# Kernel optimization log

Measured on AMD Instinct MI355X. Metric: run time of the kernel, lower is better.

Reference implementation:

```python
import jax, jax.numpy as jnp
import numpy as np

EPS = 1e-6
BETA = 0.25
NVQ_W = 1.0


def _mlp(h, params):
    # Linear + ReLU on all but last layer (dropout=0, bn=False)
    n = len(params)
    for i, (w, b) in enumerate(params):
        h = h @ w + b
        if i < n - 1:
            h = jax.nn.relu(h)
    return h


def _kuma_ab(a_raw, b_raw):
    return jax.nn.softplus(a_raw) + EPS, jax.nn.softplus(b_raw) + EPS


def _kuma_h(z, a, b):
    x = jnp.clip(jax.nn.sigmoid(z), EPS, 1.0 - EPS)
    inner = jnp.clip(1.0 - x ** a, EPS, 1.0)
    y = 1.0 - inner ** b
    return jnp.clip(y, EPS, 1.0 - EPS)


def _kuma_h_inv(y, a, b):
    y = jnp.clip(y, EPS, 1.0 - EPS)
    omy = jnp.clip(1.0 - y, EPS, 1.0)
    inner = jnp.clip(1.0 - omy ** (1.0 / b), EPS, 1.0 - EPS)
    x = jnp.clip(inner ** (1.0 / a), EPS, 1.0 - EPS)
    return jnp.log(x / (1.0 - x))


def _rq(z, codebooks):
    # Residual VQ: per level, squared-L2 nearest code (argmin), straight-through,
    # codebook + beta*commitment loss. sk_epsilon=0 -> Sinkhorn skipped.
    sg = jax.lax.stop_gradient
    residual = z
    x_q = jnp.zeros_like(z)
    losses, idx_list = [], []
    for l in range(codebooks.shape[0]):
        cb = codebooks[l]  # [K, D]
        d = (jnp.sum(residual * residual, -1, keepdims=True)
             + jnp.sum(cb * cb, -1)
             - 2.0 * residual @ cb.T)  # [B, K]
        idx = jnp.argmin(d, axis=-1)  # [B]
        q = cb[idx]  # [B, D]
        codebook_loss = jnp.mean((q - sg(residual)) ** 2)
        commit_loss = jnp.mean((sg(q) - residual) ** 2)
        losses.append(codebook_loss + BETA * commit_loss)
        q_st = residual + sg(q - residual)  # straight-through
        residual = residual - q_st
        x_q = x_q + q_st
        idx_list.append(idx)
    return x_q, jnp.mean(jnp.stack(losses)), jnp.stack(idx_list, axis=-1)


def _forward(x, enc, dec, codebooks, a_raw, b_raw):
    z = _mlp(x, enc)
    a, b = _kuma_ab(a_raw, b_raw)
    z_prime = _kuma_h(z, a, b)
    zq_prime, rq_loss, indices = _rq(z_prime, codebooks)
    z_q = _kuma_h_inv(zq_prime, a, b)
    z_recon = _kuma_h_inv(z_prime, a, b)
    nvq_loss = jnp.mean((z_recon - z) ** 2)
    total_quant_loss = rq_loss + NVQ_W * nvq_loss
    out = _mlp(z_q, dec)
    return out, total_quant_loss, indices


def setup_inputs() -> dict:
    key = jax.random.key(0)
    ks = jax.random.split(key, 16)
    B, IN = 16384, 768
    enc_dims = [768, 2048, 1024, 512, 128]
    dec_dims = enc_dims[::-1]

    def lin(k, din, dout):
        w = jax.random.normal(k, (din, dout), jnp.float32) * (1.0 / np.sqrt(din))
        return w, jnp.zeros((dout,), jnp.float32)

    inp = {"x": jax.random.normal(ks[0], (B, IN), jnp.float32)}
    for i in range(4):
        w, b = lin(ks[1 + i], enc_dims[i], enc_dims[i + 1])
        inp[f"enc_w{i}"], inp[f"enc_b{i}"] = w, b
        w, b = lin(ks[5 + i], dec_dims[i], dec_dims[i + 1])
        inp[f"dec_w{i}"], inp[f"dec_b{i}"] = w, b
    inp["codebooks"] = jax.random.normal(ks[9], (4, 256, 128), jnp.float32)
    inp["a_raw"] = jnp.zeros((128,), jnp.float32)
    inp["b_raw"] = jnp.zeros((128,), jnp.float32)
    return inp


def reference(x, enc_w0, enc_b0, enc_w1, enc_b1, enc_w2, enc_b2, enc_w3, enc_b3,
              dec_w0, dec_b0, dec_w1, dec_b1, dec_w2, dec_b2, dec_w3, dec_b3,
              codebooks, a_raw, b_raw):
    enc = [(enc_w0, enc_b0), (enc_w1, enc_b1), (enc_w2, enc_b2), (enc_w3, enc_b3)]
    dec = [(dec_w0, dec_b0), (dec_w1, dec_b1), (dec_w2, dec_b2), (dec_w3, dec_b3)]
    return _forward(x, enc, dec, codebooks, a_raw, b_raw)
```

## Files before the change

kernel.cpp:

```cpp
#include <hip/hip_runtime.h>
#include <math.h>

#define EPS_F 1e-6f
#define ONE_M_EPS (1.0f - 1e-6f)

typedef __attribute__((ext_vector_type(8))) short s16x8;
typedef __attribute__((ext_vector_type(8))) _Float16 f16x8;
typedef __attribute__((ext_vector_type(4))) float f32x4;

__device__ __forceinline__ ushort f2bf(float f) {
    union { float f; unsigned u; } v; v.f = f;
    unsigned u = v.u;
    return (ushort)((u + 0x7FFFu + ((u >> 16) & 1u)) >> 16);
}
__device__ __forceinline__ float bf2f(ushort h) {
    union { unsigned u; float f; } v; v.u = ((unsigned)h) << 16;
    return v.f;
}
__device__ __forceinline__ void split2h(float x, ushort& h, ushort& m) {
    union { _Float16 f; ushort u; } a, b;
    a.f = (_Float16)x;
    float r = x - (float)a.f;
    b.f = (_Float16)r;
    h = a.u; m = b.u;
}

#define GLL16(srcp, dstp)                                                     \
    __builtin_amdgcn_global_load_lds(                                         \
        (const __attribute__((address_space(1))) void*)(srcp),                \
        (__attribute__((address_space(3))) void*)(dstp), 16, 0, 0)

__device__ __forceinline__ int swz_k(int row, int k) { return k ^ ((row >> 1) & 3); }

template<bool RELU, int OUT2>
__global__ __launch_bounds__(256) void gemm_mfma_split2(
    const ushort* __restrict__ Ah, const ushort* __restrict__ Am,
    const ushort* __restrict__ Wh, const ushort* __restrict__ Wm,
    const float* __restrict__ bias,
    void* __restrict__ C0, void* __restrict__ C1,
    int M, int N, int K)
{
    __shared__ __align__(16) ushort As[2][2][128 * 32];
    __shared__ __align__(16) ushort Bs[2][2][128 * 32];

    const int tid  = threadIdx.x;
    const int lane = tid & 63;
    const int w    = tid >> 6;
    const int wm   = (w >> 1) * 64;
    const int wn   = (w & 1) * 64;
    const int bm   = blockIdx.x * 128;
    const int bn   = blockIdx.y * 128;

    f32x4 acc[4][4];
#pragma unroll
    for (int i = 0; i < 4; i++)
#pragma unroll
        for (int j = 0; j < 4; j++) acc[i][j] = f32x4{0.f, 0.f, 0.f, 0.f};

    const int c0 = (w * 2) * 64 + lane;
    const int c1 = (w * 2 + 1) * 64 + lane;
    const int r0 = c0 >> 2, k0e = swz_k(r0, c0 & 3) * 8;
    const int r1 = c1 >> 2, k1e = swz_k(r1, c1 & 3) * 8;

    const size_t a_off0 = (size_t)(bm + r0) * K + k0e;
    const size_t a_off1 = (size_t)(bm + r1) * K + k1e;
    const size_t b_off0 = (size_t)(bn + r0) * K + k0e;
    const size_t b_off1 = (size_t)(bn + r1) * K + k1e;
    const int d0 = (w * 2) * 512;
    const int d1 = d0 + 512;

    const ushort* Ap[2] = {Ah, Am};
    const ushort* Wp[2] = {Wh, Wm};

    const int fm  = lane & 15;
    const int fkb = lane >> 4;
    const int NT  = K >> 5;

#pragma unroll
    for (int p = 0; p < 2; p++) {
        GLL16(Ap[p] + a_off0, &As[0][p][d0]);
        GLL16(Ap[p] + a_off1, &As[0][p][d1]);
        GLL16(Wp[p] + b_off0, &Bs[0][p][d0]);
        GLL16(Wp[p] + b_off1, &Bs[0][p][d1]);
    }

    int cur = 0;
    for (int kt = 0; kt < NT; kt++) {
        if (kt + 1 < NT) {
            const int kk = (kt + 1) << 5;
#pragma unroll
            for (int p = 0; p < 2; p++) {
                GLL16(Ap[p] + a_off0 + kk, &As[cur ^ 1][p][d0]);
                GLL16(Ap[p] + a_off1 + kk, &As[cur ^ 1][p][d1]);
                GLL16(Wp[p] + b_off0 + kk, &Bs[cur ^ 1][p][d0]);
                GLL16(Wp[p] + b_off1 + kk, &Bs[cur ^ 1][p][d1]);
            }
            asm volatile("s_waitcnt vmcnt(8)" ::: "memory");
        } else {
            asm volatile("s_waitcnt vmcnt(0)" ::: "memory");
        }
        __builtin_amdgcn_s_barrier();
        asm volatile("" ::: "memory");

        f16x8 af[2][4];
#pragma unroll
        for (int p = 0; p < 2; p++)
#pragma unroll
            for (int i = 0; i < 4; i++) {
                const int row = wm + i * 16 + fm;
                af[p][i] = *reinterpret_cast<const f16x8*>(
                    &As[cur][p][row * 32 + swz_k(row, fkb) * 8]);
            }
        f16x8 bf0[4], bf1[4];
#pragma unroll
        for (int j = 0; j < 4; j++) {
            const int row = wn + j * 16 + fm;
            bf0[j] = *reinterpret_cast<const f16x8*>(&Bs[cur][0][row * 32 + swz_k(row, fkb) * 8]);
            bf1[j] = *reinterpret_cast<const f16x8*>(&Bs[cur][1][row * 32 + swz_k(row, fkb) * 8]);
        }

        __builtin_amdgcn_s_setprio(1);
#pragma unroll
        for (int i = 0; i < 4; i++)
#pragma unroll
            for (int j = 0; j < 4; j++) {
                acc[i][j] = __builtin_amdgcn_mfma_f32_16x16x32_f16(af[0][i], bf0[j], acc[i][j], 0, 0, 0);
                acc[i][j] = __builtin_amdgcn_mfma_f32_16x16x32_f16(af[0][i], bf1[j], acc[i][j], 0, 0, 0);
                acc[i][j] = __builtin_amdgcn_mfma_f32_16x16x32_f16(af[1][i], bf0[j], acc[i][j], 0, 0, 0);
            }
        __builtin_amdgcn_s_setprio(0);
        asm volatile("" ::: "memory");
        __builtin_amdgcn_s_barrier();
        cur ^= 1;
    }

#pragma unroll
    for (int j = 0; j < 4; j++) {
        const int coln = bn + wn + j * 16 + fm;
        const float bv = bias[coln];
#pragma unroll
        for (int i = 0; i < 4; i++) {
            const int row0 = bm + wm + i * 16 + (lane >> 4) * 4;
#pragma unroll
            for (int r = 0; r < 4; r++) {
                float o = acc[i][j][r] + bv;
                if (RELU) o = fmaxf(o, 0.f);
                const size_t idx = (size_t)(row0 + r) * N + coln;
                if (OUT2) {
                    ushort h, m;
                    split2h(o, h, m);
                    ((ushort*)C0)[idx] = h;
                    ((ushort*)C1)[idx] = m;
                } else {
                    ((float*)C0)[idx] = o;
                }
            }
        }
    }
}

template<bool RELU, bool OUT_BF16>
__global__ __launch_bounds__(256) void gemm_mfma_bt(
    const ushort* __restrict__ A, const ushort* __restrict__ WT,
    const float* __restrict__ bias, void* __restrict__ Cv,
    int M, int N, int K)
{
    __shared__ __align__(16) ushort As[2][128 * 32];
    __shared__ __align__(16) ushort Bs[2][128 * 32];

    const int tid  = threadIdx.x;
    const int lane = tid & 63;
    const int w    = tid >> 6;
    const int wm   = (w >> 1) * 64;
    const int wn   = (w & 1) * 64;
    const int bm   = blockIdx.x * 128;
    const int bn   = blockIdx.y * 128;

    f32x4 acc[4][4];
#pragma unroll
    for (int i = 0; i < 4; i++)
#pragma unroll
        for (int j = 0; j < 4; j++) acc[i][j] = f32x4{0.f, 0.f, 0.f, 0.f};

    const int c0 = (w * 2) * 64 + lane;
    const int c1 = (w * 2 + 1) * 64 + lane;
    const int r0 = c0 >> 2, k0e = swz_k(r0, c0 & 3) * 8;
    const int r1 = c1 >> 2, k1e = swz_k(r1, c1 & 3) * 8;

    const ushort* a_src0 = A  + (size_t)(bm + r0) * K + k0e;
    const ushort* a_src1 = A  + (size_t)(bm + r1) * K + k1e;
    const ushort* b_src0 = WT + (size_t)(bn + r0) * K + k0e;
    const ushort* b_src1 = WT + (size_t)(bn + r1) * K + k1e;
    const int d0 = (w * 2) * 512;
    const int d1 = d0 + 512;

    const int fm  = lane & 15;
    const int fkb = lane >> 4;
    const int NT  = K >> 5;

    GLL16(a_src0, &As[0][d0]);
    GLL16(a_src1, &As[0][d1]);
    GLL16(b_src0, &Bs[0][d0]);
    GLL16(b_src1, &Bs[0][d1]);

    int cur = 0;
    for (int kt = 0; kt < NT; kt++) {
        if (kt + 1 < NT) {
            const int kk = (kt + 1) << 5;
            GLL16(a_src0 + kk, &As[cur ^ 1][d0]);
            GLL16(a_src1 + kk, &As[cur ^ 1][d1]);
            GLL16(b_src0 + kk, &Bs[cur ^ 1][d0]);
            GLL16(b_src1 + kk, &Bs[cur ^ 1][d1]);
            asm volatile("s_waitcnt vmcnt(4)" ::: "memory");
        } else {
            asm volatile("s_waitcnt vmcnt(0)" ::: "memory");
        }
        __builtin_amdgcn_s_barrier();
        asm volatile("" ::: "memory");

        s16x8 af[4], bfr[4];
#pragma unroll
        for (int i = 0; i < 4; i++) {
            const int row = wm + i * 16 + fm;
            af[i] = *reinterpret_cast<const s16x8*>(&As[cur][row * 32 + swz_k(row, fkb) * 8]);
        }
#pragma unroll
        for (int j = 0; j < 4; j++) {
            const int row = wn + j * 16 + fm;
            bfr[j] = *reinterpret_cast<const s16x8*>(&Bs[cur][row * 32 + swz_k(row, fkb) * 8]);
        }

        __builtin_amdgcn_s_setprio(1);
#pragma unroll
        for (int i = 0; i < 4; i++)
#pragma unroll
            for (int j = 0; j < 4; j++)
                acc[i][j] = __builtin_amdgcn_mfma_f32_16x16x32_bf16(
                    af[i], bfr[j], acc[i][j], 0, 0, 0);
        __builtin_amdgcn_s_setprio(0);
        asm volatile("" ::: "memory");
        __builtin_amdgcn_s_barrier();
        cur ^= 1;
    }

#pragma unroll
    for (int j = 0; j < 4; j++) {
        const int coln = bn + wn + j * 16 + fm;
        const float bv = bias[coln];
#pragma unroll
        for (int i = 0; i < 4; i++) {
            const int row0 = bm + wm + i * 16 + (lane >> 4) * 4;
#pragma unroll
            for (int r = 0; r < 4; r++) {
                float o = acc[i][j][r] + bv;
                if (RELU) o = fmaxf(o, 0.f);
                if (OUT_BF16)
                    ((ushort*)Cv)[(size_t)(row0 + r) * N + coln] = f2bf(o);
                else
                    ((float*)Cv)[(size_t)(row0 + r) * N + coln] = o;
            }
        }
    }
}

__global__ __launch_bounds__(256) void transpose_to_bf16(
    const float* __restrict__ W, ushort* __restrict__ WT, int K, int N)
{
    __shared__ float t[32][33];
    const int kb = blockIdx.x * 32, nb = blockIdx.y * 32;
    const int tx = threadIdx.x & 31, ty = threadIdx.x >> 5;
#pragma unroll
    for (int i = ty; i < 32; i += 8)
        t[i][tx] = W[(size_t)(kb + i) * N + nb + tx];
    __syncthreads();
#pragma unroll
    for (int i = ty; i < 32; i += 8)
        WT[(size_t)(nb + i) * K + kb + tx] = f2bf(t[tx][i]);
}

__global__ __launch_bounds__(256) void transpose_split_f16(
    const float* __restrict__ W, ushort* __restrict__ TH,
    ushort* __restrict__ TM, int K, int N)
{
    __shared__ float t[32][33];
    const int kb = blockIdx.x * 32, nb = blockIdx.y * 32;
    const int tx = threadIdx.x & 31, ty = threadIdx.x >> 5;
#pragma unroll
    for (int i = ty; i < 32; i += 8)
        t[i][tx] = W[(size_t)(kb + i) * N + nb + tx];
    __syncthreads();
#pragma unroll
    for (int i = ty; i < 32; i += 8) {
        ushort h, m;
        split2h(t[tx][i], h, m);
        const size_t idx = (size_t)(nb + i) * K + kb + tx;
        TH[idx] = h; TM[idx] = m;
    }
}

__global__ __launch_bounds__(256) void split_plane2_kernel(
    const float* __restrict__ X, ushort* __restrict__ H,
    ushort* __restrict__ M, size_t n)
{
    size_t i = (size_t)blockIdx.x * 256 + threadIdx.x;
    if (i >= n) return;
    ushort h, m;
    split2h(X[i], h, m);
    H[i] = h; M[i] = m;
}

__global__ __launch_bounds__(128) void prep_cb_kernel(
    const float* __restrict__ cb, float* __restrict__ cbT, float* __restrict__ cnorm)
{
    int b = blockIdx.x;
    int d = threadIdx.x;
    float v = cb[(size_t)b * 128 + d];
    int l = b >> 8, c = b & 255;
    cbT[((size_t)l * 128 + d) * 256 + c] = v;
    float s = v * v;
#pragma unroll
    for (int off = 32; off > 0; off >>= 1) s += __shfl_down(s, off);
    __shared__ float ps[2];
    if ((d & 63) == 0) ps[d >> 6] = s;
    __syncthreads();
    if (d == 0) cnorm[b] = ps[0] + ps[1];
}

__device__ __forceinline__ float softplusf(float x) {
    return (x > 20.f) ? x : log1pf(expf(x));
}

__global__ void kuma_ab_init(const float* __restrict__ a_raw, const float* __restrict__ b_raw,
                             float* __restrict__ kp)
{
    int t = threadIdx.x;
    if (t < 128) {
        float a = softplusf(a_raw[t]) + EPS_F;
        float b = softplusf(b_raw[t]) + EPS_F;
        kp[t] = a;
        kp[128 + t] = b;
        kp[256 + t] = 1.f / a;
        kp[384 + t] = 1.f / b;
    }
}

__global__ __launch_bounds__(256) void kuma_h_kernel(
    const float* __restrict__ z, const float* __restrict__ kp,
    float* __restrict__ zp, int n)
{
    int i = blockIdx.x * 256 + threadIdx.x;
    if (i >= n) return;
    int col = i & 127;
    float a = kp[col], b = kp[128 + col];
    float zv = z[i];
    float x = 1.f / (1.f + expf(-zv));
    x = fminf(fmaxf(x, EPS_F), ONE_M_EPS);
    float inner = 1.f - powf(x, a);
    inner = fminf(fmaxf(inner, EPS_F), 1.f);
    float y = 1.f - powf(inner, b);
    y = fminf(fmaxf(y, EPS_F), ONE_M_EPS);
    zp[i] = y;
}

__global__ __launch_bounds__(64) void rq_kernel2(
    const float* __restrict__ zp, const float* __restrict__ cb,
    const float* __restrict__ cbT, const float* __restrict__ cnorm,
    float* __restrict__ xq, float* __restrict__ idx_out,
    float* __restrict__ prq, int bid0, int nRq)
{
    __shared__ float res[4][128];

    const int t = threadIdx.x;
    const int row0 = blockIdx.x * 4;

#pragma unroll
    for (int j = 0; j < 8; j++) {
        int e = t + j * 64;
        res[e >> 7][e & 127] = zp[(size_t)row0 * 128 + e];
    }

    float lsum[4];

#pragma unroll 1
    for (int l = 0; l < 4; l++) {
        const float* cT = cbT + (size_t)l * 32768;

        float acc[4][4];
#pragma unroll
        for (int r = 0; r < 4; r++)
#pragma unroll
            for (int cc = 0; cc < 4; cc++) acc[r][cc] = 0.f;

        float pc[16];
#pragma unroll
        for (int dd = 0; dd < 4; dd++)
#pragma unroll
            for (int cc = 0; cc < 4; cc++)
                pc[dd * 4 + cc] = cT[dd * 256 + cc * 64 + t];

#pragma unroll 2
        for (int d = 0; d < 128; d += 4) {
            float nc[16];
            if (d < 124) {
#pragma unroll
                for (int dd = 0; dd < 4; dd++)
#pragma unroll
                    for (int cc = 0; cc < 4; cc++)
                        nc[dd * 4 + cc] = cT[(d + 4 + dd) * 256 + cc * 64 + t];
            }
#pragma unroll
            for (int r = 0; r < 4; r++) {
                float4 rv = *reinterpret_cast<const float4*>(&res[r][d]);
#pragma unroll
                for (int cc = 0; cc < 4; cc++) {
                    acc[r][cc] += rv.x * pc[cc] + rv.y * pc[4 + cc]
                                + rv.z * pc[8 + cc] + rv.w * pc[12 + cc];
                }
            }
#pragma unroll
            for (int k = 0; k < 16; k++) pc[k] = nc[k];
        }

        float cn[4];
#pragma unroll
        for (int cc = 0; cc < 4; cc++) cn[cc] = cnorm[l * 256 + cc * 64 + t];

        int bidx0, bidx1, bidx2, bidx3;
#pragma unroll
        for (int r = 0; r < 4; r++) {
            float dmin = cn[0] - 2.f * acc[r][0];
            int imin = t;
#pragma unroll
            for (int cc = 1; cc < 4; cc++) {
                float dv = cn[cc] - 2.f * acc[r][cc];
                if (dv < dmin) { dmin = dv; imin = cc * 64 + t; }
            }
#pragma unroll
            for (int off = 1; off < 64; off <<= 1) {
                float d2 = __shfl_xor(dmin, off);
                int i2 = __shfl_xor(imin, off);
                if (d2 < dmin || (d2 == dmin && i2 < imin)) { dmin = d2; imin = i2; }
            }
            if (r == 0) bidx0 = imin;
            else if (r == 1) bidx1 = imin;
            else if (r == 2) bidx2 = imin;
            else bidx3 = imin;
            if (t == 0) idx_out[(size_t)(row0 + r) * 4 + l] = (float)imin;
        }

        float s = 0.f;
#pragma unroll
        for (int j = 0; j < 8; j++) {
            const int r = j >> 1;
            const int d = (j & 1) * 64 + t;
            const int bi = (r == 0) ? bidx0 : (r == 1) ? bidx1 : (r == 2) ? bidx2 : bidx3;
            float q = cb[((size_t)(l * 256) + bi) * 128 + d];
            float nr = res[r][d] - q;
            res[r][d] = nr;
            s += nr * nr;
        }
        lsum[l] = s;
    }

#pragma unroll
    for (int j = 0; j < 8; j++) {
        int e = t + j * 64;
        xq[(size_t)row0 * 128 + e] = zp[(size_t)row0 * 128 + e] - res[e >> 7][e & 127];
    }

#pragma unroll
    for (int l = 0; l < 4; l++) {
        float s = lsum[l];
#pragma unroll
        for (int off = 32; off > 0; off >>= 1) s += __shfl_down(s, off);
        if (t == 0) prq[(size_t)l * nRq + bid0 + blockIdx.x] = s;
    }
}

__device__ __forceinline__ float kuma_h_inv_f(float y, float ia, float ib) {
    y = fminf(fmaxf(y, EPS_F), ONE_M_EPS);
    float omy = fminf(fmaxf(1.f - y, EPS_F), 1.f);
    float inner = fminf(fmaxf(1.f - powf(omy, ib), EPS_F), ONE_M_EPS);
    float x = fminf(fmaxf(powf(inner, ia), EPS_F), ONE_M_EPS);
    return logf(x / (1.f - x));
}

__global__ __launch_bounds__(256) void zq_nvq_kernel(
    const float* __restrict__ xq, const float* __restrict__ zp,
    const float* __restrict__ z, const float* __restrict__ kp,
    float* __restrict__ zq, ushort* __restrict__ zq16,
    float* __restrict__ pnvq, int bid0, int n)
{
    int i = blockIdx.x * 256 + threadIdx.x;
    float ds = 0.f;
    if (i < n) {
        int col = i & 127;
        float ia = kp[256 + col], ib = kp[384 + col];
        float xv = xq[i];
        float zpv = zp[i];
        float zv = z[i];
        float zr = kuma_h_inv_f(zpv, ia, ib);
        float d = zr - zv;
        ds = d * d;
        float zqv = kuma_h_inv_f(xv, ia, ib);
        zq[i] = zqv;
        zq16[i] = f2bf(zqv);
    }
#pragma unroll
    for (int off = 32; off > 0; off >>= 1) ds += __shfl_down(ds, off);
    __shared__ float ps[4];
    if ((threadIdx.x & 63) == 0) ps[threadIdx.x >> 6] = ds;
    __syncthreads();
    if (threadIdx.x == 0)
        pnvq[bid0 + blockIdx.x] = ps[0] + ps[1] + ps[2] + ps[3];
}

__global__ __launch_bounds__(256) void finalize_kernel(
    const float* __restrict__ prq, const float* __restrict__ pnvq,
    int nRqAll, int nNvq, float* __restrict__ out_loss)
{
    const int t = threadIdx.x;
    float srq = 0.f, snvq = 0.f;
    for (int i = t; i < nRqAll; i += 256) srq += prq[i];
    for (int i = t; i < nNvq; i += 256) snvq += pnvq[i];
#pragma unroll
    for (int off = 32; off > 0; off >>= 1) {
        srq += __shfl_down(srq, off);
        snvq += __shfl_down(snvq, off);
    }
    __shared__ float pr[4], pn[4];
    if ((t & 63) == 0) { pr[t >> 6] = srq; pn[t >> 6] = snvq; }
    __syncthreads();
    if (t == 0) {
        const float inv = 1.f / (16384.f * 128.f);
        float rq = (pr[0] + pr[1] + pr[2] + pr[3]);
        float nv = (pn[0] + pn[1] + pn[2] + pn[3]);
        out_loss[0] = 0.3125f * rq * inv + nv * inv;
    }
}

extern "C" void kernel_launch(void* const* d_in, const int* in_sizes, int n_in,
                              void* d_out, int out_size, void* d_ws, size_t ws_size,
                              hipStream_t stream)
{
    constexpr int B = 16384;

    const float* x = (const float*)d_in[0];
    const float* enc_w[4]; const float* enc_b[4];
    const float* dec_w[4]; const float* dec_b[4];
    for (int i = 0; i < 4; i++) {
        enc_w[i] = (const float*)d_in[1 + 4 * i];
        enc_b[i] = (const float*)d_in[2 + 4 * i];
        dec_w[i] = (const float*)d_in[3 + 4 * i];
        dec_b[i] = (const float*)d_in[4 + 4 * i];
    }
    const float* cb    = (const float*)d_in[17];
    const float* a_raw = (const float*)d_in[18];
    const float* b_raw = (const float*)d_in[19];

    size_t avail = ws_size / 4;
    const size_t fixed_f = 6547008;
    int R = 16384;
    while (R > 256 && (size_t)R * 3520 + fixed_f > avail) R >>= 1;

    float* ws    = (float*)d_ws;
    float* slotA = ws;
    float* slotB = slotA + (size_t)R * 1024;
    float* zb    = slotB + (size_t)R * 2048;
    float* zpb   = zb  + (size_t)R * 128;
    float* xqb   = zpb + (size_t)R * 128;
    float* zq16f = xqb + (size_t)R * 128;
    float* fixp  = zq16f + (size_t)R * 64;

    ushort* ew = (ushort*)fixp;
    ushort* e0h = ew;            ushort* e0m = e0h + 1572864;
    ushort* e1h = e0m + 1572864; ushort* e1m = e1h + 2097152;
    ushort* e2h = e1m + 2097152; ushort* e2m = e2h + 524288;
    ushort* e3h = e2m + 524288;  ushort* e3m = e3h + 65536;
    ushort* wt0 = e3m + 65536;
    ushort* wt1 = wt0 + 65536;
    ushort* wt2 = wt1 + 524288;
    ushort* wt3 = wt2 + 2097152;
    float* cbT   = (float*)(wt3 + 1572864);
    float* cnorm = cbT + 4 * 128 * 256;
    float* kp    = cnorm + 4 * 256;
    float* prq   = kp + 512;
    float* pnvq  = prq + 16384;

    ushort* zq16 = (ushort*)zq16f;

    ushort* xH  = (ushort*)slotA;  ushort* xM  = xH  + (size_t)R * 768;
    ushort* h0H = (ushort*)slotB;  ushort* h0M = h0H + (size_t)R * 2048;
    ushort* h1H = (ushort*)slotA;  ushort* h1M = h1H + (size_t)R * 1024;
    ushort* h2H = (ushort*)slotB;  ushort* h2M = h2H + (size_t)R * 512;

    ushort* dA = (ushort*)slotB;
    ushort* dB = (ushort*)(slotB + (size_t)R * 256);
    ushort* dC = (ushort*)slotA;

    float* out      = (float*)d_out;
    float* out_loss = out + (size_t)B * 768;
    float* out_idx  = out_loss + 1;

    prep_cb_kernel<<<1024, 128, 0, stream>>>(cb, cbT, cnorm);
    kuma_ab_init<<<1, 128, 0, stream>>>(a_raw, b_raw, kp);
    transpose_split_f16<<<dim3( 768/32, 2048/32), 256, 0, stream>>>(enc_w[0], e0h, e0m,  768, 2048);
    transpose_split_f16<<<dim3(2048/32, 1024/32), 256, 0, stream>>>(enc_w[1], e1h, e1m, 2048, 1024);
    transpose_split_f16<<<dim3(1024/32,  512/32), 256, 0, stream>>>(enc_w[2], e2h, e2m, 1024,  512);
    transpose_split_f16<<<dim3( 512/32,  128/32), 256, 0, stream>>>(enc_w[3], e3h, e3m,  512,  128);
    transpose_to_bf16<<<dim3(128/32,  512/32), 256, 0, stream>>>(dec_w[0], wt0,  128,  512);
    transpose_to_bf16<<<dim3(512/32, 1024/32), 256, 0, stream>>>(dec_w[1], wt1,  512, 1024);
    transpose_to_bf16<<<dim3(1024/32,2048/32), 256, 0, stream>>>(dec_w[2], wt2, 1024, 2048);
    transpose_to_bf16<<<dim3(2048/32, 768/32), 256, 0, stream>>>(dec_w[3], wt3, 2048,  768);

    const int nc = B / R;
    const int nRq = B / 4;
    const int rqPerChunk = R / 4;
    const int nvqPerChunk = (R * 128) / 256;
    for (int c = 0; c < nc; c++) {
        const size_t base = (size_t)c * R;
        const float* xc = x + base * 768;
        float* outc = out + base * 768;
        float* idxc = out_idx + base * 4;

        {
            size_t n = (size_t)R * 768;
            split_plane2_kernel<<<(unsigned)((n + 255) / 256), 256, 0, stream>>>(xc, xH, xM, n);
        }

        gemm_mfma_split2<true , 1><<<dim3(R/128, 16), 256, 0, stream>>>(
            xH, xM, e0h, e0m, enc_b[0], h0H, h0M, R, 2048, 768);
        gemm_mfma_split2<true , 1><<<dim3(R/128,  8), 256, 0, stream>>>(
            h0H, h0M, e1h, e1m, enc_b[1], h1H, h1M, R, 1024, 2048);
        gemm_mfma_split2<true , 1><<<dim3(R/128,  4), 256, 0, stream>>>(
            h1H, h1M, e2h, e2m, enc_b[2], h2H, h2M, R,  512, 1024);
        gemm_mfma_split2<false, 0><<<dim3(R/128,  1), 256, 0, stream>>>(
            h2H, h2M, e3h, e3m, enc_b[3], zb, nullptr, R, 128, 512);

        kuma_h_kernel<<<(R * 128) / 256, 256, 0, stream>>>(zb, kp, zpb, R * 128);
        rq_kernel2<<<rqPerChunk, 64, 0, stream>>>(zpb, cb, cbT, cnorm, xqb, idxc,
                                                  prq, c * rqPerChunk, nRq);
        zq_nvq_kernel<<<nvqPerChunk, 256, 0, stream>>>(xqb, zpb, zb, kp, xqb, zq16,
                                                       pnvq, c * nvqPerChunk, R * 128);

        gemm_mfma_bt<true , true ><<<dim3(R/128,  4), 256, 0, stream>>>(zq16, wt0, dec_b[0], dA, R,  512,  128);
        gemm_mfma_bt<true , true ><<<dim3(R/128,  8), 256, 0, stream>>>(dA,   wt1, dec_b[1], dB, R, 1024,  512);
        gemm_mfma_bt<true , true ><<<dim3(R/128, 16), 256, 0, stream>>>(dB,   wt2, dec_b[2], dC, R, 2048, 1024);
        gemm_mfma_bt<false, false><<<dim3(R/128,  6), 256, 0, stream>>>(dC,   wt3, dec_b[3], outc, R,  768, 2048);
    }

    finalize_kernel<<<1, 256, 0, stream>>>(prq, pnvq, 4 * nRq, B * 128 / 256, out_loss);
}
```

Baseline: 913.5 us.

## Add triple-buffered 128x256 pipelined GEMM for encoder and decoder layers

```diff
diff --git a/kernel.cpp b/kernel.cpp
--- a/kernel.cpp
+++ b/kernel.cpp
@@ -31,6 +31,170 @@
         (__attribute__((address_space(3))) void*)(dstp), 16, 0, 0)
 
 __device__ __forceinline__ int swz_k(int row, int k) { return k ^ ((row >> 1) & 3); }
+
+template<int NWAIT> __device__ __forceinline__ void vmwait() {
+    if constexpr (NWAIT == 12)      asm volatile("s_waitcnt vmcnt(12)" ::: "memory");
+    else if constexpr (NWAIT == 6)  asm volatile("s_waitcnt vmcnt(6)"  ::: "memory");
+    else if constexpr (NWAIT == 3)  asm volatile("s_waitcnt vmcnt(3)"  ::: "memory");
+    else                            asm volatile("s_waitcnt vmcnt(0)"  ::: "memory");
+}
+
+template<int PLANES, bool RELU, int OUTMODE>
+__global__ __launch_bounds__(512) void gemm_pipe(
+    const ushort* __restrict__ A0, const ushort* __restrict__ A1,
+    const ushort* __restrict__ W0, const ushort* __restrict__ W1,
+    const float* __restrict__ bias,
+    void* __restrict__ C0, void* __restrict__ C1,
+    int M, int N, int K)
+{
+    __shared__ __align__(16) ushort As[3][PLANES][4096];
+    __shared__ __align__(16) ushort Bs[3][PLANES][8192];
+
+    const int tid  = threadIdx.x;
+    const int lane = tid & 63;
+    const int w    = tid >> 6;
+    const int wm   = (w >> 2) * 64;
+    const int wn   = (w & 3) * 64;
+    const int bm   = blockIdx.x * 128;
+    const int bn   = blockIdx.y * 256;
+
+    f32x4 acc[4][4];
+#pragma unroll
+    for (int i = 0; i < 4; i++)
+#pragma unroll
+        for (int j = 0; j < 4; j++) acc[i][j] = f32x4{0.f, 0.f, 0.f, 0.f};
+
+    const int sr   = tid >> 2;
+    const int skc  = swz_k(sr, tid & 3) * 8;
+    const int br1r = 128 + sr;
+    const int bk1  = swz_k(br1r, tid & 3) * 8;
+
+    const size_t a_off  = (size_t)(bm + sr)   * K + skc;
+    const size_t b_off0 = (size_t)(bn + sr)   * K + skc;
+    const size_t b_off1 = (size_t)(bn + br1r) * K + bk1;
+    const int ud = w * 512;
+
+    const ushort* Ap[2] = {A0, A1};
+    const ushort* Wp[2] = {W0, W1};
+
+    const int fm  = lane & 15;
+    const int fkb = lane >> 4;
+    const int NT  = K >> 5;
+
+    auto STAGE = [&](int kk, int b) {
+#pragma unroll
+        for (int p = 0; p < PLANES; p++) {
+            GLL16(Ap[p] + a_off  + kk, &As[b][p][ud]);
+            GLL16(Wp[p] + b_off0 + kk, &Bs[b][p][ud]);
+            GLL16(Wp[p] + b_off1 + kk, &Bs[b][p][4096 + ud]);
+        }
+    };
+
+    STAGE(0, 0);
+    STAGE(32, 1);
+
+    int cur = 0;
+    for (int kt = 0; kt < NT; kt++) {
+        __builtin_amdgcn_s_barrier();
+        asm volatile("" ::: "memory");
+        if (kt + 2 < NT) {
+            const int sb = (cur == 0) ? 2 : cur - 1;
+            STAGE((kt + 2) << 5, sb);
+            vmwait<6 * PLANES>();
+        } else if (kt + 1 < NT) {
+            vmwait<3 * PLANES>();
+        } else {
+            vmwait<0>();
+        }
+        asm volatile("" ::: "memory");
+
+        if constexpr (PLANES == 2) {
+            f16x8 a[2][4], b[2][4];
+#pragma unroll
+            for (int p = 0; p < 2; p++)
+#pragma unroll
+                for (int i = 0; i < 4; i++) {
+                    const int row = wm + i * 16 + fm;
+                    a[p][i] = *reinterpret_cast<const f16x8*>(
+                        &As[cur][p][row * 32 + swz_k(row, fkb) * 8]);
+                }
+#pragma unroll
+            for (int p = 0; p < 2; p++)
+#pragma unroll
+                for (int j = 0; j < 4; j++) {
+                    const int row = wn + j * 16 + fm;
+                    b[p][j] = *reinterpret_cast<const f16x8*>(
+                        &Bs[cur][p][row * 32 + swz_k(row, fkb) * 8]);
+                }
+            __builtin_amdgcn_s_setprio(1);
+#pragma unroll
+            for (int i = 0; i < 4; i++)
+#pragma unroll
+                for (int j = 0; j < 4; j++)
+                    acc[i][j] = __builtin_amdgcn_mfma_f32_16x16x32_f16(a[0][i], b[0][j], acc[i][j], 0, 0, 0);
+#pragma unroll
+            for (int i = 0; i < 4; i++)
+#pragma unroll
+                for (int j = 0; j < 4; j++)
+                    acc[i][j] = __builtin_amdgcn_mfma_f32_16x16x32_f16(a[0][i], b[1][j], acc[i][j], 0, 0, 0);
+#pragma unroll
+            for (int i = 0; i < 4; i++)
+#pragma unroll
+                for (int j = 0; j < 4; j++)
+                    acc[i][j] = __builtin_amdgcn_mfma_f32_16x16x32_f16(a[1][i], b[0][j], acc[i][j], 0, 0, 0);
+            __builtin_amdgcn_s_setprio(0);
+        } else {
+            s16x8 a[4], b[4];
+#pragma unroll
+            for (int i = 0; i < 4; i++) {
+                const int row = wm + i * 16 + fm;
+                a[i] = *reinterpret_cast<const s16x8*>(
+                    &As[cur][0][row * 32 + swz_k(row, fkb) * 8]);
+            }
+#pragma unroll
+            for (int j = 0; j < 4; j++) {
+                const int row = wn + j * 16 + fm;
+                b[j] = *reinterpret_cast<const s16x8*>(
+                    &Bs[cur][0][row * 32 + swz_k(row, fkb) * 8]);
+            }
+            __builtin_amdgcn_s_setprio(1);
+#pragma unroll
+            for (int i = 0; i < 4; i++)
+#pragma unroll
+                for (int j = 0; j < 4; j++)
+                    acc[i][j] = __builtin_amdgcn_mfma_f32_16x16x32_bf16(a[i], b[j], acc[i][j], 0, 0, 0);
+            __builtin_amdgcn_s_setprio(0);
+        }
+        asm volatile("" ::: "memory");
+        cur = (cur == 2) ? 0 : cur + 1;
+    }
+
+#pragma unroll
+    for (int j = 0; j < 4; j++) {
+        const int coln = bn + wn + j * 16 + fm;
+        const float bv = bias[coln];
+#pragma unroll
+        for (int i = 0; i < 4; i++) {
+            const int row0 = bm + wm + i * 16 + (lane >> 4) * 4;
+#pragma unroll
+            for (int r = 0; r < 4; r++) {
+                float o = acc[i][j][r] + bv;
+                if (RELU) o = fmaxf(o, 0.f);
+                const size_t idx = (size_t)(row0 + r) * N + coln;
+                if constexpr (OUTMODE == 1) {
+                    ushort h, m;
+                    split2h(o, h, m);
+                    ((ushort*)C0)[idx] = h;
+                    ((ushort*)C1)[idx] = m;
+                } else if constexpr (OUTMODE == 2) {
+                    ((ushort*)C0)[idx] = f2bf(o);
+                } else {
+                    ((float*)C0)[idx] = o;
+                }
+            }
+        }
+    }
+}
 
 template<bool RELU, int OUT2>
 __global__ __launch_bounds__(256) void gemm_mfma_split2(
@@ -154,110 +318,6 @@
                 } else {
                     ((float*)C0)[idx] = o;
                 }
-            }
-        }
-    }
-}
-
-template<bool RELU, bool OUT_BF16>
-__global__ __launch_bounds__(256) void gemm_mfma_bt(
-    const ushort* __restrict__ A, const ushort* __restrict__ WT,
-    const float* __restrict__ bias, void* __restrict__ Cv,
-    int M, int N, int K)
-{
-    __shared__ __align__(16) ushort As[2][128 * 32];
-    __shared__ __align__(16) ushort Bs[2][128 * 32];
-
-    const int tid  = threadIdx.x;
-    const int lane = tid & 63;
-    const int w    = tid >> 6;
-    const int wm   = (w >> 1) * 64;
-    const int wn   = (w & 1) * 64;
-    const int bm   = blockIdx.x * 128;
-    const int bn   = blockIdx.y * 128;
-
-    f32x4 acc[4][4];
-#pragma unroll
-    for (int i = 0; i < 4; i++)
-#pragma unroll
-        for (int j = 0; j < 4; j++) acc[i][j] = f32x4{0.f, 0.f, 0.f, 0.f};
-
-    const int c0 = (w * 2) * 64 + lane;
-    const int c1 = (w * 2 + 1) * 64 + lane;
-    const int r0 = c0 >> 2, k0e = swz_k(r0, c0 & 3) * 8;
-    const int r1 = c1 >> 2, k1e = swz_k(r1, c1 & 3) * 8;
-
-    const ushort* a_src0 = A  + (size_t)(bm + r0) * K + k0e;
-    const ushort* a_src1 = A  + (size_t)(bm + r1) * K + k1e;
-    const ushort* b_src0 = WT + (size_t)(bn + r0) * K + k0e;
-    const ushort* b_src1 = WT + (size_t)(bn + r1) * K + k1e;
-    const int d0 = (w * 2) * 512;
-    const int d1 = d0 + 512;
-
-    const int fm  = lane & 15;
-    const int fkb = lane >> 4;
-    const int NT  = K >> 5;
-
-    GLL16(a_src0, &As[0][d0]);
-    GLL16(a_src1, &As[0][d1]);
-    GLL16(b_src0, &Bs[0][d0]);
-    GLL16(b_src1, &Bs[0][d1]);
-
-    int cur = 0;
-    for (int kt = 0; kt < NT; kt++) {
-        if (kt + 1 < NT) {
-            const int kk = (kt + 1) << 5;
-            GLL16(a_src0 + kk, &As[cur ^ 1][d0]);
-            GLL16(a_src1 + kk, &As[cur ^ 1][d1]);
-            GLL16(b_src0 + kk, &Bs[cur ^ 1][d0]);
-            GLL16(b_src1 + kk, &Bs[cur ^ 1][d1]);
-            asm volatile("s_waitcnt vmcnt(4)" ::: "memory");
-        } else {
-            asm volatile("s_waitcnt vmcnt(0)" ::: "memory");
-        }
-        __builtin_amdgcn_s_barrier();
-        asm volatile("" ::: "memory");
-
-        s16x8 af[4], bfr[4];
-#pragma unroll
-        for (int i = 0; i < 4; i++) {
-            const int row = wm + i * 16 + fm;
-            af[i] = *reinterpret_cast<const s16x8*>(&As[cur][row * 32 + swz_k(row, fkb) * 8]);
-        }
-#pragma unroll
-        for (int j = 0; j < 4; j++) {
-            const int row = wn + j * 16 + fm;
-            bfr[j] = *reinterpret_cast<const s16x8*>(&Bs[cur][row * 32 + swz_k(row, fkb) * 8]);
-        }
-
-        __builtin_amdgcn_s_setprio(1);
-#pragma unroll
-        for (int i = 0; i < 4; i++)
-#pragma unroll
-            for (int j = 0; j < 4; j++)
-                acc[i][j] = __builtin_amdgcn_mfma_f32_16x16x32_bf16(
-                    af[i], bfr[j], acc[i][j], 0, 0, 0);
-        __builtin_amdgcn_s_setprio(0);
-        asm volatile("" ::: "memory");
-        __builtin_amdgcn_s_barrier();
-        cur ^= 1;
-    }
-
-#pragma unroll
-    for (int j = 0; j < 4; j++) {
-        const int coln = bn + wn + j * 16 + fm;
-        const float bv = bias[coln];
-#pragma unroll
-        for (int i = 0; i < 4; i++) {
-            const int row0 = bm + wm + i * 16 + (lane >> 4) * 4;
-#pragma unroll
-            for (int r = 0; r < 4; r++) {
-                float o = acc[i][j][r] + bv;
-                if (RELU) o = fmaxf(o, 0.f);
-                if (OUT_BF16)
-                    ((ushort*)Cv)[(size_t)(row0 + r) * N + coln] = f2bf(o);
-                else
-                    ((float*)Cv)[(size_t)(row0 + r) * N + coln] = o;
             }
         }
     }
@@ -628,13 +688,13 @@
             split_plane2_kernel<<<(unsigned)((n + 255) / 256), 256, 0, stream>>>(xc, xH, xM, n);
         }
 
-        gemm_mfma_split2<true , 1><<<dim3(R/128, 16), 256, 0, stream>>>(
+        gemm_pipe<2, true, 1><<<dim3(R/128, 8), 512, 0, stream>>>(
             xH, xM, e0h, e0m, enc_b[0], h0H, h0M, R, 2048, 768);
-        gemm_mfma_split2<true , 1><<<dim3(R/128,  8), 256, 0, stream>>>(
+        gemm_pipe<2, true, 1><<<dim3(R/128, 4), 512, 0, stream>>>(
             h0H, h0M, e1h, e1m, enc_b[1], h1H, h1M, R, 1024, 2048);
-        gemm_mfma_split2<true , 1><<<dim3(R/128,  4), 256, 0, stream>>>(
-            h1H, h1M, e2h, e2m, enc_b[2], h2H, h2M, R,  512, 1024);
-        gemm_mfma_split2<false, 0><<<dim3(R/128,  1), 256, 0, stream>>>(
+        gemm_pipe<2, true, 1><<<dim3(R/128, 2), 512, 0, stream>>>(
+            h1H, h1M, e2h, e2m, enc_b[2], h2H, h2M, R, 512, 1024);
+        gemm_mfma_split2<false, 0><<<dim3(R/128, 1), 256, 0, stream>>>(
             h2H, h2M, e3h, e3m, enc_b[3], zb, nullptr, R, 128, 512);
 
         kuma_h_kernel<<<(R * 128) / 256, 256, 0, stream>>>(zb, kp, zpb, R * 128);
@@ -643,10 +703,14 @@
         zq_nvq_kernel<<<nvqPerChunk, 256, 0, stream>>>(xqb, zpb, zb, kp, xqb, zq16,
                                                        pnvq, c * nvqPerChunk, R * 128);
 
-        gemm_mfma_bt<true , true ><<<dim3(R/128,  4), 256, 0, stream>>>(zq16, wt0, dec_b[0], dA, R,  512,  128);
-        gemm_mfma_bt<true , true ><<<dim3(R/128,  8), 256, 0, stream>>>(dA,   wt1, dec_b[1], dB, R, 1024,  512);
-        gemm_mfma_bt<true , true ><<<dim3(R/128, 16), 256, 0, stream>>>(dB,   wt2, dec_b[2], dC, R, 2048, 1024);
-        gemm_mfma_bt<false, false><<<dim3(R/128,  6), 256, 0, stream>>>(dC,   wt3, dec_b[3], outc, R,  768, 2048);
+        gemm_pipe<1, true, 2><<<dim3(R/128, 2), 512, 0, stream>>>(
+            zq16, nullptr, wt0, nullptr, dec_b[0], dA, nullptr, R, 512, 128);
+        gemm_pipe<1, true, 2><<<dim3(R/128, 4), 512, 0, stream>>>(
+            dA, nullptr, wt1, nullptr, dec_b[1], dB, nullptr, R, 1024, 512);
+        gemm_pipe<1, true, 2><<<dim3(R/128, 8), 512, 0, stream>>>(
+            dB, nullptr, wt2, nullptr, dec_b[2], dC, nullptr, R, 2048, 1024);
+        gemm_pipe<1, false, 0><<<dim3(R/128, 3), 512, 0, stream>>>(
+            dC, nullptr, wt3, nullptr, dec_b[3], outc, nullptr, R, 768, 2048);
     }
 
     finalize_kernel<<<1, 256, 0, stream>>>(prq, pnvq, 4 * nRq, B * 128 / 256, out_loss);
```

Result: slower. 939.0 us (+2.8%).

## Remap GEMM tile order for cache locality and double RQ rows per block

Applied to the files above, without the earlier changes.

```diff
diff --git a/kernel.cpp b/kernel.cpp
--- a/kernel.cpp
+++ b/kernel.cpp
@@ -31,6 +31,24 @@
         (__attribute__((address_space(3))) void*)(dstp), 16, 0, 0)
 
 __device__ __forceinline__ int swz_k(int row, int k) { return k ^ ((row >> 1) & 3); }
+
+__device__ __forceinline__ void tile_remap(int MB, int NB, int& bm_i, int& bn_i) {
+    const int lin = blockIdx.y * MB + blockIdx.x;
+    const int nwg = MB * NB;
+    int wg = lin;
+    if ((nwg & 7) == 0)
+        wg = (lin & 7) * (nwg >> 3) + (lin >> 3);
+    if (((MB | NB) & 1) == 0) {
+        const int tiles_m = MB >> 1;
+        const int stile = wg >> 2, within = wg & 3;
+        const int st_m = stile % tiles_m, st_n = stile / tiles_m;
+        bm_i = st_m * 2 + (within & 1);
+        bn_i = st_n * 2 + (within >> 1);
+    } else {
+        bm_i = wg % MB;
+        bn_i = wg / MB;
+    }
+}
 
 template<bool RELU, int OUT2>
 __global__ __launch_bounds__(256) void gemm_mfma_split2(
@@ -48,8 +66,10 @@
     const int w    = tid >> 6;
     const int wm   = (w >> 1) * 64;
     const int wn   = (w & 1) * 64;
-    const int bm   = blockIdx.x * 128;
-    const int bn   = blockIdx.y * 128;
+    int bmi, bni;
+    tile_remap(gridDim.x, gridDim.y, bmi, bni);
+    const int bm   = bmi * 128;
+    const int bn   = bni * 128;
 
     f32x4 acc[4][4];
 #pragma unroll
@@ -173,8 +193,10 @@
     const int w    = tid >> 6;
     const int wm   = (w >> 1) * 64;
     const int wn   = (w & 1) * 64;
-    const int bm   = blockIdx.x * 128;
-    const int bn   = blockIdx.y * 128;
+    int bmi, bni;
+    tile_remap(gridDim.x, gridDim.y, bmi, bni);
+    const int bm   = bmi * 128;
+    const int bn   = bni * 128;
 
     f32x4 acc[4][4];
 #pragma unroll
@@ -362,32 +384,33 @@
     zp[i] = y;
 }
 
-__global__ __launch_bounds__(64) void rq_kernel2(
+__global__ __launch_bounds__(64) void rq_kernel3(
     const float* __restrict__ zp, const float* __restrict__ cb,
     const float* __restrict__ cbT, const float* __restrict__ cnorm,
     float* __restrict__ xq, float* __restrict__ idx_out,
     float* __restrict__ prq, int bid0, int nRq)
 {
-    __shared__ float res[4][128];
+    __shared__ float res[8][128];
 
     const int t = threadIdx.x;
-    const int row0 = blockIdx.x * 4;
-
-#pragma unroll
-    for (int j = 0; j < 8; j++) {
+    const int row0 = blockIdx.x * 8;
+
+#pragma unroll
+    for (int j = 0; j < 16; j++) {
         int e = t + j * 64;
         res[e >> 7][e & 127] = zp[(size_t)row0 * 128 + e];
     }
 
     float lsum[4];
+    int bidx[8];
 
 #pragma unroll 1
     for (int l = 0; l < 4; l++) {
         const float* cT = cbT + (size_t)l * 32768;
 
-        float acc[4][4];
-#pragma unroll
-        for (int r = 0; r < 4; r++)
+        float acc[8][4];
+#pragma unroll
+        for (int r = 0; r < 8; r++)
 #pragma unroll
             for (int cc = 0; cc < 4; cc++) acc[r][cc] = 0.f;
 
@@ -409,7 +432,7 @@
                         nc[dd * 4 + cc] = cT[(d + 4 + dd) * 256 + cc * 64 + t];
             }
 #pragma unroll
-            for (int r = 0; r < 4; r++) {
+            for (int r = 0; r < 8; r++) {
                 float4 rv = *reinterpret_cast<const float4*>(&res[r][d]);
 #pragma unroll
                 for (int cc = 0; cc < 4; cc++) {
@@ -425,9 +448,8 @@
 #pragma unroll
         for (int cc = 0; cc < 4; cc++) cn[cc] = cnorm[l * 256 + cc * 64 + t];
 
-        int bidx0, bidx1, bidx2, bidx3;
-#pragma unroll
-        for (int r = 0; r < 4; r++) {
+#pragma unroll
+        for (int r = 0; r < 8; r++) {
             float dmin = cn[0] - 2.f * acc[r][0];
             int imin = t;
 #pragma unroll
@@ -441,20 +463,16 @@
                 int i2 = __shfl_xor(imin, off);
                 if (d2 < dmin || (d2 == dmin && i2 < imin)) { dmin = d2; imin = i2; }
             }
-            if (r == 0) bidx0 = imin;
-            else if (r == 1) bidx1 = imin;
-            else if (r == 2) bidx2 = imin;
-            else bidx3 = imin;
+            bidx[r] = imin;
             if (t == 0) idx_out[(size_t)(row0 + r) * 4 + l] = (float)imin;
         }
 
         float s = 0.f;
 #pragma unroll
-        for (int j = 0; j < 8; j++) {
+        for (int j = 0; j < 16; j++) {
             const int r = j >> 1;
             const int d = (j & 1) * 64 + t;
-            const int bi = (r == 0) ? bidx0 : (r == 1) ? bidx1 : (r == 2) ? bidx2 : bidx3;
-            float q = cb[((size_t)(l * 256) + bi) * 128 + d];
+            float q = cb[((size_t)(l * 256) + bidx[r]) * 128 + d];
             float nr = res[r][d] - q;
             res[r][d] = nr;
             s += nr * nr;
@@ -463,7 +481,7 @@
     }
 
 #pragma unroll
-    for (int j = 0; j < 8; j++) {
+    for (int j = 0; j < 16; j++) {
         int e = t + j * 64;
         xq[(size_t)row0 * 128 + e] = zp[(size_t)row0 * 128 + e] - res[e >> 7][e & 127];
     }
@@ -614,8 +632,8 @@
     transpose_to_bf16<<<dim3(2048/32, 768/32), 256, 0, stream>>>(dec_w[3], wt3, 2048,  768);
 
     const int nc = B / R;
-    const int nRq = B / 4;
-    const int rqPerChunk = R / 4;
+    const int nRq = B / 8;
+    const int rqPerChunk = R / 8;
     const int nvqPerChunk = (R * 128) / 256;
     for (int c = 0; c < nc; c++) {
         const size_t base = (size_t)c * R;
@@ -638,7 +656,7 @@
             h2H, h2M, e3h, e3m, enc_b[3], zb, nullptr, R, 128, 512);
 
         kuma_h_kernel<<<(R * 128) / 256, 256, 0, stream>>>(zb, kp, zpb, R * 128);
-        rq_kernel2<<<rqPerChunk, 64, 0, stream>>>(zpb, cb, cbT, cnorm, xqb, idxc,
+        rq_kernel3<<<rqPerChunk, 64, 0, stream>>>(zpb, cb, cbT, cnorm, xqb, idxc,
                                                   prq, c * rqPerChunk, nRq);
         zq_nvq_kernel<<<nvqPerChunk, 256, 0, stream>>>(xqb, zpb, zb, kp, xqb, zq16,
                                                        pnvq, c * nvqPerChunk, R * 128);
```

Measured after the change: 874.9 us, median of 2. -4.2%, faster.
